# Performance work log

Hardware: AMD Instinct MI355X
Metric: run time of the kernel (lower is better)

Reference implementation:

```python
import jax, jax.numpy as jnp
import numpy as np

N_NODES = 100000
D = 64


def setup_inputs() -> dict:
    key = jax.random.key(0)
    ks = jax.random.split(key, 8)
    x = jax.random.normal(ks[0], (N_NODES, D), dtype=jnp.float32)
    edge_index = jax.random.randint(ks[1], (2, 1000000), 0, N_NODES, dtype=jnp.int64)
    s = 1.0 / np.sqrt(D)
    W0 = jax.random.uniform(ks[2], (D, D), jnp.float32, -s, s)
    W1 = jax.random.uniform(ks[3], (D, D), jnp.float32, -s, s)
    W2 = jax.random.uniform(ks[4], (D, D), jnp.float32, -s, s)
    b0 = jnp.zeros((D,), jnp.float32)
    b1 = jnp.zeros((D,), jnp.float32)
    b2 = jnp.zeros((D,), jnp.float32)
    return {"x": x, "edge_index": edge_index,
            "W0": W0, "b0": b0, "W1": W1, "b1": b1, "W2": W2, "b2": b2}


def _gcn_layer(x, src, dst, norm, W, b):
    # GCNConv: h = D^{-1/2}(A+I)D^{-1/2} (x W) + b
    h = x @ W                                   # [N, D_out]
    msg = h[src] * norm[:, None]                # gather + scale, [E', D_out]
    agg = jax.ops.segment_sum(msg, dst, num_segments=x.shape[0])
    return jax.nn.relu(agg + b)


def reference(x, edge_index, W0, b0, W1, b1, W2, b2):
    n = x.shape[0]
    # add self loops (GCNConv default add_self_loops=True)
    loops = jnp.arange(n, dtype=edge_index.dtype)
    src = jnp.concatenate([edge_index[0], loops])
    dst = jnp.concatenate([edge_index[1], loops])
    # symmetric normalization deg^{-1/2}[src] * deg^{-1/2}[dst]
    deg = jax.ops.segment_sum(jnp.ones_like(src, dtype=x.dtype), dst, num_segments=n)
    dinv = jnp.where(deg > 0, jax.lax.rsqrt(deg), 0.0)
    norm = dinv[src] * dinv[dst]                # [E']
    # dropout p=0.0 / eval mode -> identity
    h = _gcn_layer(x, src, dst, norm, W0, b0)
    h = _gcn_layer(h, src, dst, norm, W1, b1)
    h = _gcn_layer(h, src, dst, norm, W2, b2)
    return h
```

## Files before the change

### kernel.cpp

```cpp
#include <hip/hip_runtime.h>
#include <hip/hip_fp16.h>

#define N_NODES 100000
#define CAP 64
#define NB  391
#define BE  2048

typedef _Float16 v4h __attribute__((ext_vector_type(4)));
typedef float    v4f __attribute__((ext_vector_type(4)));


__global__ __launch_bounds__(256) void k_bucket(
    const int* __restrict__ src, const int* __restrict__ dst, int E, int NBLK,
    unsigned int* __restrict__ arr, unsigned short* __restrict__ scantab,
    const float* __restrict__ W0, const float* __restrict__ W1,
    const float* __restrict__ W2,
    __half* __restrict__ Wt0h, __half* __restrict__ Wt0l,
    __half* __restrict__ Wt1, __half* __restrict__ Wt2) {
    if ((int)blockIdx.x == NBLK) {
        for (int i = threadIdx.x; i < 4096; i += 256) {
            int k = i >> 6, c = i & 63;
            float w0 = W0[i];
            __half w0h = __float2half(w0);
            Wt0h[(c << 6) + k] = w0h;
            Wt0l[(c << 6) + k] = __float2half(w0 - __half2float(w0h));
            Wt1[(c << 6) + k] = __float2half(W1[i]);
            Wt2[(c << 6) + k] = __float2half(W2[i]);
        }
        return;
    }
    __shared__ int cnt[392];
    __shared__ int scn[392];
    __shared__ int gs[98];
    __shared__ unsigned int lsort[BE];
    int t = threadIdx.x;
    for (int j = t; j < 392; j += 256) cnt[j] = 0;
    __syncthreads();
    int blk = blockIdx.x;
    int base = blk * BE;
    int dsts[8], srcs[8], rnk[8];
#pragma unroll
    for (int i = 0; i < 8; i++) {
        int e = base + i * 256 + t;
        int d = (e < E) ? dst[e] : -1;
        srcs[i] = (e < E) ? src[e] : 0;
        dsts[i] = d;
        rnk[i] = (d >= 0) ? atomicAdd(&cnt[d >> 8], 1) : 0;
    }
    __syncthreads();
    int c0 = 0, c1 = 0, c2 = 0, c3 = 0;
    if (t < 98) {
        c0 = cnt[4 * t]; c1 = cnt[4 * t + 1]; c2 = cnt[4 * t + 2]; c3 = cnt[4 * t + 3];
        gs[t] = c0 + c1 + c2 + c3;
    }
    __syncthreads();
#pragma unroll
    for (int off = 1; off < 128; off <<= 1) {
        int u = (t < 98 && t >= off) ? gs[t - off] : 0;
        __syncthreads();
        if (t < 98) gs[t] += u;
        __syncthreads();
    }
    if (t < 98) {
        int b0 = gs[t] - (c0 + c1 + c2 + c3);
        scn[4 * t]     = b0;
        scn[4 * t + 1] = b0 + c0;
        scn[4 * t + 2] = b0 + c0 + c1;
        scn[4 * t + 3] = b0 + c0 + c1 + c2;
    }
    __syncthreads();
#pragma unroll
    for (int i = 0; i < 8; i++) {
        int d = dsts[i];
        if (d >= 0) {
            int pos = scn[d >> 8] + rnk[i];
            lsort[pos] = ((unsigned)(d & 255) << 17) | (unsigned)srcs[i];
        }
    }
    __syncthreads();
    uint4* ap = (uint4*)(arr + (size_t)blk * BE);
    const uint4* ls4 = (const uint4*)lsort;
#pragma unroll
    for (int i = 0; i < 2; i++) ap[t + i * 256] = ls4[t + i * 256];
    for (int j = t; j < 392; j += 256)
        scantab[(size_t)blk * 392 + j] = (unsigned short)scn[j];
}

__global__ __launch_bounds__(256) void k_build0(
    const unsigned int* __restrict__ arr,
    const unsigned short* __restrict__ scantab,
    int* __restrict__ csr, int* __restrict__ deg, int NBLK, int n,
    const float* __restrict__ x,
    const __half* __restrict__ Wth, const __half* __restrict__ Wtl,
    __half* __restrict__ outh) {
    __shared__ int4 lcsr4[4096];
    __shared__ int cnt[256];
    __shared__ _Float16 xs_hi[16 * 68];
    __shared__ _Float16 xs_lo[16 * 68];
    int* lcsr = (int*)lcsr4;
    int t = threadIdx.x;
    cnt[t] = 0;
    __syncthreads();
    int b = blockIdx.x;
    int bn = b << 8;
    for (int blk = t; blk < NBLK; blk += 256) {
        int s0 = scantab[(size_t)blk * 392 + b];
        int s1 = scantab[(size_t)blk * 392 + b + 1];
        const unsigned int* a = arr + (size_t)blk * BE;
        for (int k = s0; k < s1; k++) {
            unsigned v = a[k];
            int dloc = (int)(v >> 17);
            int sv = (int)(v & 0x1FFFF);
            int r = atomicAdd(&cnt[dloc], 1);
            if (r < CAP) lcsr[(dloc << 6) + r] = sv;
        }
    }
    __syncthreads();
    int rows = min(256, n - bn);
    int4* cdst = (int4*)(csr + ((size_t)bn << 6));
    for (int i = t; i < rows * 16; i += 256) cdst[i] = lcsr4[i];
    if (bn + t < n) deg[bn + t] = cnt[t];
    int rl = t >> 4, q = t & 15;
    int lane = t & 63;
    int w = t >> 6;
    int col = (w << 4) + (lane & 15);
    int g = lane >> 4;
    const v4h* wth4 = (const v4h*)(Wth + ((size_t)col << 6));
    const v4h* wtl4 = (const v4h*)(Wtl + ((size_t)col << 6));
    v4h bfh[4], bfl[4];
#pragma unroll
    for (int s = 0; s < 4; s++) { bfh[s] = wth4[(s << 2) + g]; bfl[s] = wtl4[(s << 2) + g]; }

    int tiles = rows >> 4;
    v4f xv = __builtin_nontemporal_load((const v4f*)x + (size_t)bn * 16 + t);
    for (int it = 0; it < tiles; it++) {
        int nb16 = bn + it * 16;
        v4h yh = {(_Float16)xv.x, (_Float16)xv.y, (_Float16)xv.z, (_Float16)xv.w};
        v4h yl = {(_Float16)(xv.x - (float)yh.x), (_Float16)(xv.y - (float)yh.y),
                  (_Float16)(xv.z - (float)yh.z), (_Float16)(xv.w - (float)yh.w)};
        *(v4h*)&xs_hi[rl * 68 + (q << 2)] = yh;
        *(v4h*)&xs_lo[rl * 68 + (q << 2)] = yl;
        v4f xn = xv;
        if (it + 1 < tiles)
            xn = __builtin_nontemporal_load(
                (const v4f*)x + (size_t)(nb16 + 16) * 16 + t);
        __syncthreads();
        v4f acc = {0.f, 0.f, 0.f, 0.f};
        int arow = lane & 15;
#pragma unroll
        for (int s = 0; s < 4; s++) {
            v4h al = *(const v4h*)&xs_lo[arow * 68 + (s << 4) + (g << 2)];
            v4h ah = *(const v4h*)&xs_hi[arow * 68 + (s << 4) + (g << 2)];
            acc = __builtin_amdgcn_mfma_f32_16x16x16f16(al, bfh[s], acc, 0, 0, 0);
            acc = __builtin_amdgcn_mfma_f32_16x16x16f16(ah, bfl[s], acc, 0, 0, 0);
            acc = __builtin_amdgcn_mfma_f32_16x16x16f16(ah, bfh[s], acc, 0, 0, 0);
        }
#pragma unroll
        for (int j = 0; j < 4; j++) {
            int r = (g << 2) + j;
            float dr = rsqrtf((float)(cnt[it * 16 + r] + 1));
            float v = acc[j] * dr;
            outh[((size_t)(nb16 + r) << 6) + col] = __float2half(v);
        }
        __syncthreads();
        xv = xn;
    }
}


__device__ __forceinline__ uint4 padd4(uint4 u, uint4 v) {
    __half2* a = (__half2*)&u;
    __half2* b = (__half2*)&v;
    uint4 r;
    __half2* c = (__half2*)&r;
#pragma unroll
    for (int k = 0; k < 4; k++) c[k] = __hadd2(a[k], b[k]);
    return r;
}

__device__ __forceinline__ void acc_h4(v4f& A, v4f& B, uint4 v) {
    __half2* h = (__half2*)&v;
    float2 f0 = __half22float2(h[0]);
    float2 f1 = __half22float2(h[1]);
    float2 f2 = __half22float2(h[2]);
    float2 f3 = __half22float2(h[3]);
    v4f fa = {f0.x, f0.y, f1.x, f1.y};
    v4f fb = {f2.x, f2.y, f3.x, f3.y};
    A = A + fa;
    B = B + fb;
}

__device__ __forceinline__ void gather_acc4(const uint4* __restrict__ h4,
                                            const int* __restrict__ csr,
                                            int4 ia, int4 ib,
                                            int node, int qq, int cnt,
                                            v4f& yA, v4f& yB) {
    const int4* c4 = (const int4*)(csr + (node << 6));
    v4f A0 = {0,0,0,0}, A1 = {0,0,0,0}, A2 = {0,0,0,0}, A3 = {0,0,0,0};
    v4f B0 = {0,0,0,0}, B1 = {0,0,0,0}, B2 = {0,0,0,0}, B3 = {0,0,0,0};
    acc_h4(A0, B0, h4[(size_t)node * 8 + qq]);
    int e = 0;
    for (; e + 8 <= cnt; ) {
        uint4 v0 = h4[(size_t)ia.x * 8 + qq];
        uint4 v1 = h4[(size_t)ia.y * 8 + qq];
        uint4 v2 = h4[(size_t)ia.z * 8 + qq];
        uint4 v3 = h4[(size_t)ia.w * 8 + qq];
        uint4 v4 = h4[(size_t)ib.x * 8 + qq];
        uint4 v5 = h4[(size_t)ib.y * 8 + qq];
        uint4 v6 = h4[(size_t)ib.z * 8 + qq];
        uint4 v7 = h4[(size_t)ib.w * 8 + qq];
        e += 8;
        ia = c4[e >> 2];
        ib = c4[(e >> 2) + 1];
        uint4 p0 = padd4(v0, v1);
        uint4 p1 = padd4(v2, v3);
        uint4 p2 = padd4(v4, v5);
        uint4 p3 = padd4(v6, v7);
        acc_h4(A0, B0, p0); acc_h4(A1, B1, p1);
        acc_h4(A2, B2, p2); acc_h4(A3, B3, p3);
    }
    if (e + 4 <= cnt) {
        uint4 v0 = h4[(size_t)ia.x * 8 + qq];
        uint4 v1 = h4[(size_t)ia.y * 8 + qq];
        uint4 v2 = h4[(size_t)ia.z * 8 + qq];
        uint4 v3 = h4[(size_t)ia.w * 8 + qq];
        uint4 p0 = padd4(v0, v1);
        uint4 p1 = padd4(v2, v3);
        acc_h4(A1, B1, p0); acc_h4(A2, B2, p1);
        e += 4;
        ia = ib;
    }
    int rem = cnt - e;
    if (rem > 0) {
        int j0 = ia.x;
        int j1 = (rem > 1) ? ia.y : j0;
        int j2 = (rem > 2) ? ia.z : j0;
        uint4 v0 = h4[(size_t)j0 * 8 + qq];
        uint4 v1 = h4[(size_t)j1 * 8 + qq];
        uint4 v2 = h4[(size_t)j2 * 8 + qq];
        acc_h4(A1, B1, v0);
        if (rem > 1) acc_h4(A2, B2, v1);
        if (rem > 2) acc_h4(A3, B3, v2);
    }
    yA = (A0 + A1) + (A2 + A3);
    yB = (B0 + B1) + (B2 + B3);
}

__global__ __launch_bounds__(256) void k_gather_gemm(const uint4* __restrict__ h4,
                                                     const int* __restrict__ csr,
                                                     const int* __restrict__ deg,
                                                     const float* __restrict__ bias,
                                                     const __half* __restrict__ Wt,
                                                     __half* __restrict__ outh, int n) {
    __shared__ _Float16 xs_hi[32 * 68];
    __shared__ _Float16 xs_lo[32 * 68];
    __shared__ float dsv[32];
    (void)n;
    int t = threadIdx.x;
    int nl = t >> 3, qq = t & 7;
    int node = blockIdx.x * 32 + nl;
    int lane = t & 63;
    int w = t >> 6;
    int col = (w << 4) + (lane & 15);
    int g = lane >> 4;

    const int4* c4 = (const int4*)(csr + (node << 6));
    int4 ia0 = c4[0];
    int4 ib0 = c4[1];
    int dg = deg[node];
    int cnt = min(dg, CAP);
    float d_i = rsqrtf((float)(dg + 1));
    if (qq == 0) dsv[nl] = d_i;
    float4 bA = ((const float4*)bias)[qq * 2 + 0];
    float4 bB = ((const float4*)bias)[qq * 2 + 1];

    v4f aA, aB;
    gather_acc4(h4, csr, ia0, ib0, node, qq, cnt, aA, aB);

    const v4h* wt4 = (const v4h*)(Wt + ((size_t)col << 6));
    v4h bf[4];
#pragma unroll
    for (int s = 0; s < 4; s++) bf[s] = wt4[(s << 2) + g];

    float y0 = fmaxf(fmaf(aA.x, d_i, bA.x), 0.f);
    float y1 = fmaxf(fmaf(aA.y, d_i, bA.y), 0.f);
    float y2 = fmaxf(fmaf(aA.z, d_i, bA.z), 0.f);
    float y3 = fmaxf(fmaf(aA.w, d_i, bA.w), 0.f);
    float y4 = fmaxf(fmaf(aB.x, d_i, bB.x), 0.f);
    float y5 = fmaxf(fmaf(aB.y, d_i, bB.y), 0.f);
    float y6 = fmaxf(fmaf(aB.z, d_i, bB.z), 0.f);
    float y7 = fmaxf(fmaf(aB.w, d_i, bB.w), 0.f);
    v4h yhA = {(_Float16)y0, (_Float16)y1, (_Float16)y2, (_Float16)y3};
    v4h ylA = {(_Float16)(y0 - (float)yhA.x), (_Float16)(y1 - (float)yhA.y),
               (_Float16)(y2 - (float)yhA.z), (_Float16)(y3 - (float)yhA.w)};
    v4h yhB = {(_Float16)y4, (_Float16)y5, (_Float16)y6, (_Float16)y7};
    v4h ylB = {(_Float16)(y4 - (float)yhB.x), (_Float16)(y5 - (float)yhB.y),
               (_Float16)(y6 - (float)yhB.z), (_Float16)(y7 - (float)yhB.w)};
    *(v4h*)&xs_hi[nl * 68 + (qq << 3) + 0] = yhA;
    *(v4h*)&xs_hi[nl * 68 + (qq << 3) + 4] = yhB;
    *(v4h*)&xs_lo[nl * 68 + (qq << 3) + 0] = ylA;
    *(v4h*)&xs_lo[nl * 68 + (qq << 3) + 4] = ylB;
    __syncthreads();

    v4f acc0 = {0.f, 0.f, 0.f, 0.f};
    v4f acc1 = {0.f, 0.f, 0.f, 0.f};
    int ar = lane & 15;
#pragma unroll
    for (int s = 0; s < 4; s++) {
        int ko = (s << 4) + (g << 2);
        v4h al0 = *(const v4h*)&xs_lo[ar * 68 + ko];
        v4h ah0 = *(const v4h*)&xs_hi[ar * 68 + ko];
        v4h al1 = *(const v4h*)&xs_lo[(ar + 16) * 68 + ko];
        v4h ah1 = *(const v4h*)&xs_hi[(ar + 16) * 68 + ko];
        acc0 = __builtin_amdgcn_mfma_f32_16x16x16f16(al0, bf[s], acc0, 0, 0, 0);
        acc0 = __builtin_amdgcn_mfma_f32_16x16x16f16(ah0, bf[s], acc0, 0, 0, 0);
        acc1 = __builtin_amdgcn_mfma_f32_16x16x16f16(al1, bf[s], acc1, 0, 0, 0);
        acc1 = __builtin_amdgcn_mfma_f32_16x16x16f16(ah1, bf[s], acc1, 0, 0, 0);
    }

#pragma unroll
    for (int j = 0; j < 4; j++) {
        int r0 = (g << 2) + j;
        float v0 = acc0[j] * dsv[r0];
        outh[((size_t)(blockIdx.x * 32 + r0) << 6) + col] = __float2half(v0);
        int r1 = r0 + 16;
        float v1 = acc1[j] * dsv[r1];
        outh[((size_t)(blockIdx.x * 32 + r1) << 6) + col] = __float2half(v1);
    }
}

__global__ __launch_bounds__(256) void k_gather(const uint4* __restrict__ h4,
                                                const int* __restrict__ csr,
                                                const int* __restrict__ deg,
                                                const float* __restrict__ bias,
                                                float* __restrict__ out, int n) {
    int t = threadIdx.x;
    int nl = t >> 3, qq = t & 7;
    int node = blockIdx.x * 32 + nl;
    if (node >= n) return;
    const int4* c4 = (const int4*)(csr + (node << 6));
    int4 ia0 = c4[0];
    int4 ib0 = c4[1];
    int dg = deg[node];
    int cnt = min(dg, CAP);
    float d = rsqrtf((float)(dg + 1));
    v4f aA, aB;
    gather_acc4(h4, csr, ia0, ib0, node, qq, cnt, aA, aB);
    float4 bA = ((const float4*)bias)[qq * 2 + 0];
    float4 bB = ((const float4*)bias)[qq * 2 + 1];
    float4 rA, rB;
    rA.x = fmaxf(fmaf(aA.x, d, bA.x), 0.f);
    rA.y = fmaxf(fmaf(aA.y, d, bA.y), 0.f);
    rA.z = fmaxf(fmaf(aA.z, d, bA.z), 0.f);
    rA.w = fmaxf(fmaf(aA.w, d, bA.w), 0.f);
    rB.x = fmaxf(fmaf(aB.x, d, bB.x), 0.f);
    rB.y = fmaxf(fmaf(aB.y, d, bB.y), 0.f);
    rB.z = fmaxf(fmaf(aB.z, d, bB.z), 0.f);
    rB.w = fmaxf(fmaf(aB.w, d, bB.w), 0.f);
    ((float4*)out)[(size_t)node * 16 + qq * 2 + 0] = rA;
    ((float4*)out)[(size_t)node * 16 + qq * 2 + 1] = rB;
}


extern "C" void kernel_launch(void* const* d_in, const int* in_sizes, int n_in,
                              void* d_out, int out_size, void* d_ws, size_t ws_size,
                              hipStream_t stream) {
    const float* x  = (const float*)d_in[0];
    const int*   ei = (const int*)d_in[1];
    const float* W0 = (const float*)d_in[2];
    const float* b0 = (const float*)d_in[3];
    const float* W1 = (const float*)d_in[4];
    const float* b1 = (const float*)d_in[5];
    const float* W2 = (const float*)d_in[6];
    const float* b2 = (const float*)d_in[7];
    float* out = (float*)d_out;

    const int N = N_NODES;
    int E = in_sizes[1] / 2;
    const int* src = ei;
    const int* dst = ei + E;
    const int NBLK = (E + BE - 1) / BE;

    char* p = (char*)d_ws;
    auto alloc = [&](size_t bytes) -> void* {
        void* r = (void*)p;
        p += (bytes + 511) & ~(size_t)511;
        return r;
    };
    int*    deg  = (int*)alloc((size_t)N * 4);
    unsigned int*   arr     = (unsigned int*)alloc((size_t)NBLK * BE * 4);
    unsigned short* scantab = (unsigned short*)alloc((size_t)NBLK * 392 * 2);
    int*    csr  = (int*)alloc((size_t)N * CAP * 4);
    uint4*  hA   = (uint4*)alloc((size_t)N * 64 * 2);
    uint4*  hB   = (uint4*)alloc((size_t)N * 64 * 2);
    __half* Wt0h = (__half*)alloc(4096 * 2);
    __half* Wt0l = (__half*)alloc(4096 * 2);
    __half* Wt1  = (__half*)alloc(4096 * 2);
    __half* Wt2  = (__half*)alloc(4096 * 2);

    const int GATH_B = N / 32;

    k_bucket<<<NBLK + 1, 256, 0, stream>>>(src, dst, E, NBLK, arr, scantab,
                                           W0, W1, W2, Wt0h, Wt0l, Wt1, Wt2);
    k_build0<<<NB, 256, 0, stream>>>(arr, scantab, csr, deg, NBLK, N,
                                     x, Wt0h, Wt0l, (__half*)hA);
    k_gather_gemm<<<GATH_B, 256, 0, stream>>>(hA, csr, deg, b0, Wt1, (__half*)hB, N);
    k_gather_gemm<<<GATH_B, 256, 0, stream>>>(hB, csr, deg, b1, Wt2, (__half*)hA, N);
    k_gather<<<GATH_B, 256, 0, stream>>>(hA, csr, deg, b2, out, N);
}
```

Baseline: 214.2 us.

## Split fused gather-GEMM into feature-sliced gather and separate MFMA GEMM kernels

Replaces the fused gather+GEMM kernel with two kernels. A gather kernel splits the 64 features into four slices, each handled by its own block, and writes fp32 activations to a scratch buffer. A GEMM kernel then reads that buffer and applies the MFMA transform. Slicing shrinks each block's gather footprint, so gathered rows should fit better in cache. In exchange it adds two launches and an extra fp32 round trip through memory per layer, and the CSR indices are re-read for each slice.

```diff
diff --git a/kernel.cpp b/kernel.cpp
--- a/kernel.cpp
+++ b/kernel.cpp
@@ -5,6 +5,7 @@
 #define CAP 64
 #define NB  391
 #define BE  2048
+#define SLICES 4
 
 typedef _Float16 v4h __attribute__((ext_vector_type(4)));
 typedef float    v4f __attribute__((ext_vector_type(4)));
@@ -193,22 +194,22 @@
 __device__ __forceinline__ void gather_acc4(const uint4* __restrict__ h4,
                                             const int* __restrict__ csr,
                                             int4 ia, int4 ib,
-                                            int node, int qq, int cnt,
+                                            int node, int qo, int cnt,
                                             v4f& yA, v4f& yB) {
     const int4* c4 = (const int4*)(csr + (node << 6));
     v4f A0 = {0,0,0,0}, A1 = {0,0,0,0}, A2 = {0,0,0,0}, A3 = {0,0,0,0};
     v4f B0 = {0,0,0,0}, B1 = {0,0,0,0}, B2 = {0,0,0,0}, B3 = {0,0,0,0};
-    acc_h4(A0, B0, h4[(size_t)node * 8 + qq]);
+    acc_h4(A0, B0, h4[(size_t)node * 8 + qo]);
     int e = 0;
     for (; e + 8 <= cnt; ) {
-        uint4 v0 = h4[(size_t)ia.x * 8 + qq];
-        uint4 v1 = h4[(size_t)ia.y * 8 + qq];
-        uint4 v2 = h4[(size_t)ia.z * 8 + qq];
-        uint4 v3 = h4[(size_t)ia.w * 8 + qq];
-        uint4 v4 = h4[(size_t)ib.x * 8 + qq];
-        uint4 v5 = h4[(size_t)ib.y * 8 + qq];
-        uint4 v6 = h4[(size_t)ib.z * 8 + qq];
-        uint4 v7 = h4[(size_t)ib.w * 8 + qq];
+        uint4 v0 = h4[(size_t)ia.x * 8 + qo];
+        uint4 v1 = h4[(size_t)ia.y * 8 + qo];
+        uint4 v2 = h4[(size_t)ia.z * 8 + qo];
+        uint4 v3 = h4[(size_t)ia.w * 8 + qo];
+        uint4 v4 = h4[(size_t)ib.x * 8 + qo];
+        uint4 v5 = h4[(size_t)ib.y * 8 + qo];
+        uint4 v6 = h4[(size_t)ib.z * 8 + qo];
+        uint4 v7 = h4[(size_t)ib.w * 8 + qo];
         e += 8;
         ia = c4[e >> 2];
         ib = c4[(e >> 2) + 1];
@@ -220,10 +221,10 @@
         acc_h4(A2, B2, p2); acc_h4(A3, B3, p3);
     }
     if (e + 4 <= cnt) {
-        uint4 v0 = h4[(size_t)ia.x * 8 + qq];
-        uint4 v1 = h4[(size_t)ia.y * 8 + qq];
-        uint4 v2 = h4[(size_t)ia.z * 8 + qq];
-        uint4 v3 = h4[(size_t)ia.w * 8 + qq];
+        uint4 v0 = h4[(size_t)ia.x * 8 + qo];
+        uint4 v1 = h4[(size_t)ia.y * 8 + qo];
+        uint4 v2 = h4[(size_t)ia.z * 8 + qo];
+        uint4 v3 = h4[(size_t)ia.w * 8 + qo];
         uint4 p0 = padd4(v0, v1);
         uint4 p1 = padd4(v2, v3);
         acc_h4(A1, B1, p0); acc_h4(A2, B2, p1);
@@ -235,9 +236,9 @@
         int j0 = ia.x;
         int j1 = (rem > 1) ? ia.y : j0;
         int j2 = (rem > 2) ? ia.z : j0;
-        uint4 v0 = h4[(size_t)j0 * 8 + qq];
-        uint4 v1 = h4[(size_t)j1 * 8 + qq];
-        uint4 v2 = h4[(size_t)j2 * 8 + qq];
+        uint4 v0 = h4[(size_t)j0 * 8 + qo];
+        uint4 v1 = h4[(size_t)j1 * 8 + qo];
+        uint4 v2 = h4[(size_t)j2 * 8 + qo];
         acc_h4(A1, B1, v0);
         if (rem > 1) acc_h4(A2, B2, v1);
         if (rem > 2) acc_h4(A3, B3, v2);
@@ -246,98 +247,18 @@
     yB = (B0 + B1) + (B2 + B3);
 }
 
-__global__ __launch_bounds__(256) void k_gather_gemm(const uint4* __restrict__ h4,
-                                                     const int* __restrict__ csr,
-                                                     const int* __restrict__ deg,
-                                                     const float* __restrict__ bias,
-                                                     const __half* __restrict__ Wt,
-                                                     __half* __restrict__ outh, int n) {
-    __shared__ _Float16 xs_hi[32 * 68];
-    __shared__ _Float16 xs_lo[32 * 68];
-    __shared__ float dsv[32];
-    (void)n;
+__global__ __launch_bounds__(256) void k_gatherS(const uint4* __restrict__ h4,
+                                                 const int* __restrict__ csr,
+                                                 const int* __restrict__ deg,
+                                                 const float* __restrict__ bias,
+                                                 float* __restrict__ y, int n) {
     int t = threadIdx.x;
-    int nl = t >> 3, qq = t & 7;
-    int node = blockIdx.x * 32 + nl;
-    int lane = t & 63;
-    int w = t >> 6;
-    int col = (w << 4) + (lane & 15);
-    int g = lane >> 4;
-
-    const int4* c4 = (const int4*)(csr + (node << 6));
-    int4 ia0 = c4[0];
-    int4 ib0 = c4[1];
-    int dg = deg[node];
-    int cnt = min(dg, CAP);
-    float d_i = rsqrtf((float)(dg + 1));
-    if (qq == 0) dsv[nl] = d_i;
-    float4 bA = ((const float4*)bias)[qq * 2 + 0];
-    float4 bB = ((const float4*)bias)[qq * 2 + 1];
-
-    v4f aA, aB;
-    gather_acc4(h4, csr, ia0, ib0, node, qq, cnt, aA, aB);
-
-    const v4h* wt4 = (const v4h*)(Wt + ((size_t)col << 6));
-    v4h bf[4];
-#pragma unroll
-    for (int s = 0; s < 4; s++) bf[s] = wt4[(s << 2) + g];
-
-    float y0 = fmaxf(fmaf(aA.x, d_i, bA.x), 0.f);
-    float y1 = fmaxf(fmaf(aA.y, d_i, bA.y), 0.f);
-    float y2 = fmaxf(fmaf(aA.z, d_i, bA.z), 0.f);
-    float y3 = fmaxf(fmaf(aA.w, d_i, bA.w), 0.f);
-    float y4 = fmaxf(fmaf(aB.x, d_i, bB.x), 0.f);
-    float y5 = fmaxf(fmaf(aB.y, d_i, bB.y), 0.f);
-    float y6 = fmaxf(fmaf(aB.z, d_i, bB.z), 0.f);
-    float y7 = fmaxf(fmaf(aB.w, d_i, bB.w), 0.f);
-    v4h yhA = {(_Float16)y0, (_Float16)y1, (_Float16)y2, (_Float16)y3};
-    v4h ylA = {(_Float16)(y0 - (float)yhA.x), (_Float16)(y1 - (float)yhA.y),
-               (_Float16)(y2 - (float)yhA.z), (_Float16)(y3 - (float)yhA.w)};
-    v4h yhB = {(_Float16)y4, (_Float16)y5, (_Float16)y6, (_Float16)y7};
-    v4h ylB = {(_Float16)(y4 - (float)yhB.x), (_Float16)(y5 - (float)yhB.y),
-               (_Float16)(y6 - (float)yhB.z), (_Float16)(y7 - (float)yhB.w)};
-    *(v4h*)&xs_hi[nl * 68 + (qq << 3) + 0] = yhA;
-    *(v4h*)&xs_hi[nl * 68 + (qq << 3) + 4] = yhB;
-    *(v4h*)&xs_lo[nl * 68 + (qq << 3) + 0] = ylA;
-    *(v4h*)&xs_lo[nl * 68 + (qq << 3) + 4] = ylB;
-    __syncthreads();
-
-    v4f acc0 = {0.f, 0.f, 0.f, 0.f};
-    v4f acc1 = {0.f, 0.f, 0.f, 0.f};
-    int ar = lane & 15;
-#pragma unroll
-    for (int s = 0; s < 4; s++) {
-        int ko = (s << 4) + (g << 2);
-        v4h al0 = *(const v4h*)&xs_lo[ar * 68 + ko];
-        v4h ah0 = *(const v4h*)&xs_hi[ar * 68 + ko];
-        v4h al1 = *(const v4h*)&xs_lo[(ar + 16) * 68 + ko];
-        v4h ah1 = *(const v4h*)&xs_hi[(ar + 16) * 68 + ko];
-        acc0 = __builtin_amdgcn_mfma_f32_16x16x16f16(al0, bf[s], acc0, 0, 0, 0);
-        acc0 = __builtin_amdgcn_mfma_f32_16x16x16f16(ah0, bf[s], acc0, 0, 0, 0);
-        acc1 = __builtin_amdgcn_mfma_f32_16x16x16f16(al1, bf[s], acc1, 0, 0, 0);
-        acc1 = __builtin_amdgcn_mfma_f32_16x16x16f16(ah1, bf[s], acc1, 0, 0, 0);
-    }
-
-#pragma unroll
-    for (int j = 0; j < 4; j++) {
-        int r0 = (g << 2) + j;
-        float v0 = acc0[j] * dsv[r0];
-        outh[((size_t)(blockIdx.x * 32 + r0) << 6) + col] = __float2half(v0);
-        int r1 = r0 + 16;
-        float v1 = acc1[j] * dsv[r1];
-        outh[((size_t)(blockIdx.x * 32 + r1) << 6) + col] = __float2half(v1);
-    }
-}
-
-__global__ __launch_bounds__(256) void k_gather(const uint4* __restrict__ h4,
-                                                const int* __restrict__ csr,
-                                                const int* __restrict__ deg,
-                                                const float* __restrict__ bias,
-                                                float* __restrict__ out, int n) {
-    int t = threadIdx.x;
-    int nl = t >> 3, qq = t & 7;
-    int node = blockIdx.x * 32 + nl;
+    int slice = blockIdx.x & (SLICES - 1);
+    int tile  = blockIdx.x >> 2;
+    int nl = t >> 1, q2 = t & 1;
+    int node = tile * 128 + nl;
     if (node >= n) return;
+    int qo = slice * 2 + q2;
     const int4* c4 = (const int4*)(csr + (node << 6));
     int4 ia0 = c4[0];
     int4 ib0 = c4[1];
@@ -345,9 +266,9 @@
     int cnt = min(dg, CAP);
     float d = rsqrtf((float)(dg + 1));
     v4f aA, aB;
-    gather_acc4(h4, csr, ia0, ib0, node, qq, cnt, aA, aB);
-    float4 bA = ((const float4*)bias)[qq * 2 + 0];
-    float4 bB = ((const float4*)bias)[qq * 2 + 1];
+    gather_acc4(h4, csr, ia0, ib0, node, qo, cnt, aA, aB);
+    float4 bA = ((const float4*)bias)[qo * 2 + 0];
+    float4 bB = ((const float4*)bias)[qo * 2 + 1];
     float4 rA, rB;
     rA.x = fmaxf(fmaf(aA.x, d, bA.x), 0.f);
     rA.y = fmaxf(fmaf(aA.y, d, bA.y), 0.f);
@@ -357,8 +278,57 @@
     rB.y = fmaxf(fmaf(aB.y, d, bB.y), 0.f);
     rB.z = fmaxf(fmaf(aB.z, d, bB.z), 0.f);
     rB.w = fmaxf(fmaf(aB.w, d, bB.w), 0.f);
-    ((float4*)out)[(size_t)node * 16 + qq * 2 + 0] = rA;
-    ((float4*)out)[(size_t)node * 16 + qq * 2 + 1] = rB;
+    ((float4*)y)[(size_t)node * 16 + qo * 2 + 0] = rA;
+    ((float4*)y)[(size_t)node * 16 + qo * 2 + 1] = rB;
+}
+
+__global__ __launch_bounds__(256) void k_gemmY(const float* __restrict__ y,
+                                               const __half* __restrict__ Wt,
+                                               const int* __restrict__ deg,
+                                               __half* __restrict__ outh) {
+    __shared__ _Float16 xs_hi[16 * 68];
+    __shared__ _Float16 xs_lo[16 * 68];
+    __shared__ float dsv[16];
+    int t = threadIdx.x;
+    int rl = t >> 4, q = t & 15;
+    int lane = t & 63;
+    int w = t >> 6;
+    int col = (w << 4) + (lane & 15);
+    int g = lane >> 4;
+    int node = blockIdx.x * 16 + rl;
+
+    v4f xv = __builtin_nontemporal_load((const v4f*)y + (size_t)blockIdx.x * 256 + t);
+    int dg = deg[node];
+    float d_i = rsqrtf((float)(dg + 1));
+    if (q == 0) dsv[rl] = d_i;
+
+    const v4h* wt4 = (const v4h*)(Wt + ((size_t)col << 6));
+    v4h bf[4];
+#pragma unroll
+    for (int s = 0; s < 4; s++) bf[s] = wt4[(s << 2) + g];
+
+    v4h yh = {(_Float16)xv.x, (_Float16)xv.y, (_Float16)xv.z, (_Float16)xv.w};
+    v4h yl = {(_Float16)(xv.x - (float)yh.x), (_Float16)(xv.y - (float)yh.y),
+              (_Float16)(xv.z - (float)yh.z), (_Float16)(xv.w - (float)yh.w)};
+    *(v4h*)&xs_hi[rl * 68 + (q << 2)] = yh;
+    *(v4h*)&xs_lo[rl * 68 + (q << 2)] = yl;
+    __syncthreads();
+
+    v4f acc = {0.f, 0.f, 0.f, 0.f};
+    int arow = lane & 15;
+#pragma unroll
+    for (int s = 0; s < 4; s++) {
+        v4h al = *(const v4h*)&xs_lo[arow * 68 + (s << 4) + (g << 2)];
+        v4h ah = *(const v4h*)&xs_hi[arow * 68 + (s << 4) + (g << 2)];
+        acc = __builtin_amdgcn_mfma_f32_16x16x16f16(al, bf[s], acc, 0, 0, 0);
+        acc = __builtin_amdgcn_mfma_f32_16x16x16f16(ah, bf[s], acc, 0, 0, 0);
+    }
+#pragma unroll
+    for (int j = 0; j < 4; j++) {
+        int r = (g << 2) + j;
+        float v = acc[j] * dsv[r];
+        outh[((size_t)(blockIdx.x * 16 + r) << 6) + col] = __float2half(v);
+    }
 }
 
 
@@ -393,18 +363,22 @@
     int*    csr  = (int*)alloc((size_t)N * CAP * 4);
     uint4*  hA   = (uint4*)alloc((size_t)N * 64 * 2);
     uint4*  hB   = (uint4*)alloc((size_t)N * 64 * 2);
+    float*  y    = (float*)alloc((size_t)N * 64 * 4);
     __half* Wt0h = (__half*)alloc(4096 * 2);
     __half* Wt0l = (__half*)alloc(4096 * 2);
     __half* Wt1  = (__half*)alloc(4096 * 2);
     __half* Wt2  = (__half*)alloc(4096 * 2);
 
-    const int GATH_B = N / 32;
+    const int GS_B = ((N + 127) / 128) * SLICES;
+    const int GY_B = N / 16;
 
     k_bucket<<<NBLK + 1, 256, 0, stream>>>(src, dst, E, NBLK, arr, scantab,
                                            W0, W1, W2, Wt0h, Wt0l, Wt1, Wt2);
     k_build0<<<NB, 256, 0, stream>>>(arr, scantab, csr, deg, NBLK, N,
                                      x, Wt0h, Wt0l, (__half*)hA);
-    k_gather_gemm<<<GATH_B, 256, 0, stream>>>(hA, csr, deg, b0, Wt1, (__half*)hB, N);
-    k_gather_gemm<<<GATH_B, 256, 0, stream>>>(hB, csr, deg, b1, Wt2, (__half*)hA, N);
-    k_gather<<<GATH_B, 256, 0, stream>>>(hA, csr, deg, b2, out, N);
-}
+    k_gatherS<<<GS_B, 256, 0, stream>>>(hA, csr, deg, b0, y, N);
+    k_gemmY<<<GY_B, 256, 0, stream>>>(y, Wt1, deg, (__half*)hB);
+    k_gatherS<<<GS_B, 256, 0, stream>>>(hB, csr, deg, b1, y, N);
+    k_gemmY<<<GY_B, 256, 0, stream>>>(y, Wt2, deg, (__half*)hA);
+    k_gatherS<<<GS_B, 256, 0, stream>>>(hA, csr, deg, b2, out, N);
+}
```

Measured after the change: 395.7 us. 1.85x slower.
